# Kernel tuning notes

Measured on AMD Instinct MI355X. Metric: run time of the kernel, lower is better.

The kernel has to match this reference:

```python
import jax, jax.numpy as jnp
import numpy as np

N_NODES = 100000
N_EDGES = 10000
N_PAIRS = 1600000
F = 128


def setup_inputs() -> dict:
    key = jax.random.key(0)
    ks = jax.random.split(key, 7)
    x = jax.random.normal(ks[0], (N_NODES, F), dtype=jnp.float32)
    action = jax.random.uniform(ks[1], (N_NODES, 3), dtype=jnp.float32)
    W_msg = jax.random.normal(ks[2], (F, F), dtype=jnp.float32) * (1.0 / np.sqrt(F))
    W_upd = jax.random.normal(ks[3], (F, F), dtype=jnp.float32) * (1.0 / np.sqrt(F))
    b_upd = jax.random.normal(ks[4], (F,), dtype=jnp.float32) * 0.02
    pair_node = jax.random.randint(ks[5], (N_PAIRS,), 0, N_NODES, dtype=jnp.int32)
    pair_edge = jax.random.randint(ks[6], (N_PAIRS,), 0, N_EDGES, dtype=jnp.int32)
    return {"x": x, "action": action, "W_msg": W_msg, "W_upd": W_upd,
            "b_upd": b_upd, "pair_node": pair_node, "pair_edge": pair_edge}


def _v2v_mean(m, pair_node, pair_edge):
    # v2e: mean of incident node features per hyperedge, then
    # e2v: mean of incident hyperedge features per node.
    ones = jnp.ones((pair_node.shape[0],), dtype=m.dtype)
    edge_deg = jax.ops.segment_sum(ones, pair_edge, num_segments=N_EDGES)
    node_deg = jax.ops.segment_sum(ones, pair_node, num_segments=N_NODES)
    # gather node features to incidence pairs, reduce into edges  [E, F]
    e_feat = jax.ops.segment_sum(m[pair_node], pair_edge, num_segments=N_EDGES)
    e_feat = e_feat / jnp.maximum(edge_deg, 1.0)[:, None]
    # gather edge features back to pairs, reduce into nodes       [N, F]
    v_feat = jax.ops.segment_sum(e_feat[pair_edge], pair_node, num_segments=N_NODES)
    v_feat = v_feat / jnp.maximum(node_deg, 1.0)[:, None]
    return v_feat


def reference(x, action, W_msg, W_upd, b_upd, pair_node, pair_edge):
    send = action[:, 0] + action[:, 2]      # [N]
    receive = action[:, 0] + action[:, 1]   # [N]
    m_ji = x @ W_msg.T                       # lin_message (no bias)
    m_ji = jax.nn.gelu(m_ji, approximate=False)  # dropout=0 (eval)
    m_ji = m_ji * send[:, None]
    m_i = _v2v_mean(m_ji, pair_node, pair_edge)
    m_i = m_i * receive[:, None]
    h_i = jax.nn.gelu(x @ W_upd.T + b_upd + m_i, approximate=False)
    return h_i
```

## Files before the change

### kernel.cpp

```cpp
#include <hip/hip_runtime.h>

#define N_NODESC 100000
#define N_EDGESC 10000
#define N_PAIRSC 1600000
#define FDIM 128

#define NB 200
#define EPB 50
#define NPB 500
#define ECAP2 8704
#define PA_CHUNK 8192
#define PA_NCH ((N_PAIRSC + PA_CHUNK - 1) / PA_CHUNK)

typedef short bf16x8 __attribute__((ext_vector_type(8)));
typedef float f32x4 __attribute__((ext_vector_type(4)));
typedef float f32x2 __attribute__((ext_vector_type(2)));
typedef int i32x4 __attribute__((ext_vector_type(4)));
typedef unsigned u32x4 __attribute__((ext_vector_type(4)));

__device__ __forceinline__ unsigned short f2b(float f) {
  unsigned u = __float_as_uint(f);
  u += 0x7fffu + ((u >> 16) & 1u);
  return (unsigned short)(u >> 16);
}
__device__ __forceinline__ float b2f(unsigned short b) {
  return __uint_as_float(((unsigned)b) << 16);
}
__device__ __forceinline__ unsigned pack2(float a, float b) {
  return (unsigned)f2b(a) | ((unsigned)f2b(b) << 16);
}
__device__ __forceinline__ float gelu_fast(float z) {
  float z2 = z * z;
  float w = fmaf(0.044715f, z2, 1.0f);
  float e = __expf(1.5957691216f * z * w);
  return z * e * __builtin_amdgcn_rcpf(e + 1.0f);
}
__device__ __forceinline__ bf16x8 ldA(const float* p) {
  float4 u0 = *(const float4*)p;
  float4 u1 = *(const float4*)(p + 4);
  u32x4 w = {pack2(u0.x, u0.y), pack2(u0.z, u0.w), pack2(u1.x, u1.y), pack2(u1.z, u1.w)};
  return __builtin_bit_cast(bf16x8, w);
}

__global__ __launch_bounds__(256) void k_prep(const float* __restrict__ action,
                                              const float* __restrict__ wmsg, const float* __restrict__ wupd,
                                              short* __restrict__ wmsgb, short* __restrict__ wupdb,
                                              float* __restrict__ send, float* __restrict__ recv,
                                              int* __restrict__ gcure, int* __restrict__ gcurn) {
  int i = blockIdx.x * 256 + threadIdx.x;
  if (i < FDIM * FDIM) {
    wmsgb[i] = (short)f2b(wmsg[i]);
    wupdb[i] = (short)f2b(wupd[i]);
  }
  if (i < N_NODESC) {
    float a0 = action[i * 3 + 0], a1 = action[i * 3 + 1], a2 = action[i * 3 + 2];
    send[i] = a0 + a2;
    recv[i] = a0 + a1;
  }
  if (i < NB) {
    gcure[i] = i * ECAP2;
    gcurn[i] = i * ECAP2;
  }
}

__device__ __forceinline__ int wave_incl_scan(int v, int lane) {
#pragma unroll
  for (int d = 1; d < 64; d <<= 1) {
    int n = __shfl_up(v, d, 64);
    if (lane >= d) v += n;
  }
  return v;
}

__global__ __launch_bounds__(256) void k_part(const int* __restrict__ pn, const int* __restrict__ pe,
                                              int* __restrict__ gcure, int* __restrict__ gcurn,
                                              unsigned* __restrict__ buckE,
                                              unsigned* __restrict__ buckN) {
  __shared__ int ce[NB], cn[NB];
  int t = threadIdx.x;
  for (int i = t; i < NB; i += 256) { ce[i] = 0; cn[i] = 0; }
  __syncthreads();
  long long base = (long long)blockIdx.x * PA_CHUNK;
  for (int q = t; q < PA_CHUNK / 4; q += 256) {
    long long idx = base + (long long)q * 4;
    if (idx >= N_PAIRSC) break;
    i32x4 e4 = __builtin_nontemporal_load((const i32x4*)(pe + idx));
    i32x4 v4 = __builtin_nontemporal_load((const i32x4*)(pn + idx));
#pragma unroll
    for (int j = 0; j < 4; j++) {
      atomicAdd(&ce[e4[j] / EPB], 1);
      atomicAdd(&cn[v4[j] / NPB], 1);
    }
  }
  __syncthreads();
  for (int i = t; i < NB; i += 256) {
    ce[i] = atomicAdd(&gcure[i], ce[i]);
    cn[i] = atomicAdd(&gcurn[i], cn[i]);
  }
  __syncthreads();
  for (int q = t; q < PA_CHUNK / 4; q += 256) {
    long long idx = base + (long long)q * 4;
    if (idx >= N_PAIRSC) break;
    i32x4 e4 = __builtin_nontemporal_load((const i32x4*)(pe + idx));
    i32x4 v4 = __builtin_nontemporal_load((const i32x4*)(pn + idx));
#pragma unroll
    for (int j = 0; j < 4; j++) {
      unsigned ee = (unsigned)e4[j], vv = (unsigned)v4[j];
      int p1 = atomicAdd(&ce[ee / EPB], 1);
      buckE[p1] = (ee << 17) | vv;
      int p2 = atomicAdd(&cn[vv / NPB], 1);
      buckN[p2] = (vv << 14) | ee;
    }
  }
}

__global__ __launch_bounds__(256) void k_fine(const unsigned* __restrict__ buckE,
                                              const unsigned* __restrict__ buckN,
                                              const int* __restrict__ gcure, const int* __restrict__ gcurn,
                                              int* __restrict__ ecnt, int* __restrict__ eoff,
                                              int* __restrict__ ncnt, int* __restrict__ noff,
                                              int* __restrict__ sn, int* __restrict__ se) {
  __shared__ int cnt_s[NPB], cur_s[NPB];
  int b = blockIdx.x, t = threadIdx.x;
  const unsigned* buck;
  int *kcnt, *koff, *out;
  int keys, lo, beg, end, shift, mask;
  if (b < NB) {
    buck = buckE; kcnt = ecnt; koff = eoff; out = sn;
    keys = EPB; lo = b * EPB; beg = b * ECAP2; end = gcure[b];
    shift = 17; mask = 0x1FFFF;
  } else {
    int bb = b - NB;
    buck = buckN; kcnt = ncnt; koff = noff; out = se;
    keys = NPB; lo = bb * NPB; beg = bb * ECAP2; end = gcurn[bb];
    shift = 14; mask = 0x3FFF;
  }
  for (int i = t; i < keys; i += 256) cnt_s[i] = 0;
  __syncthreads();
  for (int i = beg + t; i < end; i += 256) {
    int key = (int)(buck[i] >> shift) - lo;
    atomicAdd(&cnt_s[key], 1);
  }
  __syncthreads();
  if (t < 64) {
    int carry = beg;
    for (int base = 0; base < keys; base += 64) {
      int idx = base + t;
      int v = (idx < keys) ? cnt_s[idx] : 0;
      int inc = wave_incl_scan(v, t);
      if (idx < keys) cur_s[idx] = carry + inc - v;
      carry += __shfl(inc, 63, 64);
    }
  }
  __syncthreads();
  for (int i = t; i < keys; i += 256) {
    kcnt[lo + i] = cnt_s[i];
    koff[lo + i] = cur_s[i];
  }
  __syncthreads();
  for (int i = beg + t; i < end; i += 256) {
    unsigned u = buck[i];
    int key = (int)(u >> shift) - lo;
    int val = (int)(u & mask);
    int pos = atomicAdd(&cur_s[key], 1);
    out[pos] = val;
  }
}

__global__ __launch_bounds__(256) void k_gemm_msg(const float* __restrict__ x, const short* __restrict__ wb,
                                                  const float* __restrict__ send,
                                                  unsigned char* __restrict__ mji8) {
  int gw = (blockIdx.x * 256 + threadIdx.x) >> 6;
  int lane = threadIdx.x & 63;
  if (gw >= N_NODESC / 32) return;
  int rb = gw * 32;
  int lr = lane & 15, lg = lane >> 4;

  bf16x8 A0[4], A1[4];
  const float* xrow0 = x + (size_t)(rb + lr) * FDIM + lg * 8;
  const float* xrow1 = xrow0 + 16 * FDIM;
#pragma unroll
  for (int kk = 0; kk < 4; kk++) {
    A0[kk] = ldA(xrow0 + kk * 32);
    A1[kk] = ldA(xrow1 + kk * 32);
  }

  float sv0[4], sv1[4];
#pragma unroll
  for (int j = 0; j < 4; j++) {
    sv0[j] = send[rb + lg * 4 + j];
    sv1[j] = send[rb + 16 + lg * 4 + j];
  }

#pragma unroll
  for (int c = 0; c < 8; c++) {
    f32x4 acc0 = {0.f, 0.f, 0.f, 0.f}, acc1 = {0.f, 0.f, 0.f, 0.f};
    const short* wrow = wb + (size_t)(16 * c + lr) * FDIM + lg * 8;
#pragma unroll
    for (int kk = 0; kk < 4; kk++) {
      bf16x8 B = *(const bf16x8*)(wrow + kk * 32);
      acc0 = __builtin_amdgcn_mfma_f32_16x16x32_bf16(A0[kk], B, acc0, 0, 0, 0);
      acc1 = __builtin_amdgcn_mfma_f32_16x16x32_bf16(A1[kk], B, acc1, 0, 0, 0);
    }
    int col = 16 * c + lr;
#pragma unroll
    for (int j = 0; j < 4; j++) {
      float m0 = gelu_fast(acc0[j]) * sv0[j];
      float m1 = gelu_fast(acc1[j]) * sv1[j];
      int row0 = rb + lg * 4 + j;
      mji8[(size_t)row0 * FDIM + col] =
          (unsigned char)(__builtin_amdgcn_cvt_pk_fp8_f32(m0, m0, 0, false) & 0xFF);
      mji8[(size_t)(row0 + 16) * FDIM + col] =
          (unsigned char)(__builtin_amdgcn_cvt_pk_fp8_f32(m1, m1, 0, false) & 0xFF);
    }
  }
}

__global__ __launch_bounds__(256) void k_edge(const unsigned char* __restrict__ mji8, const int* __restrict__ sn,
                                              const int* __restrict__ eoff, const int* __restrict__ ecnt,
                                              unsigned char* __restrict__ efeat8) {
  int wave = blockIdx.x * 4 + (threadIdx.x >> 6);
  int lane = threadIdx.x & 63;
  int half = lane >> 5;
  int sub2 = (lane >> 4) & 1;
  int c4 = lane & 15;
  int edge = wave * 2 + half;
  if (edge >= N_EDGESC) return;
  int beg = eoff[edge], cnt = ecnt[edge];
  f32x2 a0 = {0.f, 0.f}, a1 = {0.f, 0.f}, a2 = {0.f, 0.f}, a3 = {0.f, 0.f};
#pragma unroll 4
  for (int p = sub2; p < cnt; p += 2) {
    int node = sn[beg + p];
    uint2 u = ((const uint2*)(mji8 + (size_t)node * FDIM))[c4];
    a0 += __builtin_amdgcn_cvt_pk_f32_fp8(u.x, false);
    a1 += __builtin_amdgcn_cvt_pk_f32_fp8(u.x, true);
    a2 += __builtin_amdgcn_cvt_pk_f32_fp8(u.y, false);
    a3 += __builtin_amdgcn_cvt_pk_f32_fp8(u.y, true);
  }
  a0[0] += __shfl_xor(a0[0], 16, 64); a0[1] += __shfl_xor(a0[1], 16, 64);
  a1[0] += __shfl_xor(a1[0], 16, 64); a1[1] += __shfl_xor(a1[1], 16, 64);
  a2[0] += __shfl_xor(a2[0], 16, 64); a2[1] += __shfl_xor(a2[1], 16, 64);
  a3[0] += __shfl_xor(a3[0], 16, 64); a3[1] += __shfl_xor(a3[1], 16, 64);
  if (sub2 == 0) {
    float inv = 1.0f / fmaxf((float)cnt, 1.0f);
    uint2 o;
    o.x = (unsigned)__builtin_amdgcn_cvt_pk_fp8_f32(a0[0] * inv, a0[1] * inv, 0, false);
    o.x = (unsigned)__builtin_amdgcn_cvt_pk_fp8_f32(a1[0] * inv, a1[1] * inv, (int)o.x, true);
    o.y = (unsigned)__builtin_amdgcn_cvt_pk_fp8_f32(a2[0] * inv, a2[1] * inv, 0, false);
    o.y = (unsigned)__builtin_amdgcn_cvt_pk_fp8_f32(a3[0] * inv, a3[1] * inv, (int)o.y, true);
    ((uint2*)(efeat8 + (size_t)edge * FDIM))[c4] = o;
  }
}

__global__ __launch_bounds__(256) void k_node(const unsigned char* __restrict__ efeat8, const int* __restrict__ se,
                                              const int* __restrict__ noff, const int* __restrict__ ncnt,
                                              const float* __restrict__ recv, short* __restrict__ mi) {
  int wave = blockIdx.x * 4 + (threadIdx.x >> 6);
  int lane = threadIdx.x & 63;
  int sub = lane >> 4, c4 = lane & 15;
  int node = wave * 4 + sub;
  int beg = noff[node], cnt = ncnt[node];
  f32x2 a0 = {0.f, 0.f}, a1 = {0.f, 0.f}, a2 = {0.f, 0.f}, a3 = {0.f, 0.f};
#pragma unroll 4
  for (int p = 0; p < cnt; p++) {
    int e = se[beg + p];
    uint2 u = ((const uint2*)(efeat8 + (size_t)e * FDIM))[c4];
    a0 += __builtin_amdgcn_cvt_pk_f32_fp8(u.x, false);
    a1 += __builtin_amdgcn_cvt_pk_f32_fp8(u.x, true);
    a2 += __builtin_amdgcn_cvt_pk_f32_fp8(u.y, false);
    a3 += __builtin_amdgcn_cvt_pk_f32_fp8(u.y, true);
  }
  float s = recv[node] / fmaxf((float)cnt, 1.0f);
  u32x4 o;
  o[0] = pack2(a0[0] * s, a0[1] * s);
  o[1] = pack2(a1[0] * s, a1[1] * s);
  o[2] = pack2(a2[0] * s, a2[1] * s);
  o[3] = pack2(a3[0] * s, a3[1] * s);
  ((u32x4*)(mi + (size_t)node * FDIM))[c4] = o;
}

__global__ __launch_bounds__(256) void k_gemm_upd(const float* __restrict__ x, const short* __restrict__ wb,
                                                  const float* __restrict__ bias, const short* __restrict__ mi,
                                                  float* __restrict__ out) {
  int gw = (blockIdx.x * 256 + threadIdx.x) >> 6;
  int lane = threadIdx.x & 63;
  if (gw >= N_NODESC / 32) return;
  int rb = gw * 32;
  int lr = lane & 15, lg = lane >> 4;

  bf16x8 A0[4], A1[4];
  const float* xrow0 = x + (size_t)(rb + lr) * FDIM + lg * 8;
  const float* xrow1 = xrow0 + 16 * FDIM;
#pragma unroll
  for (int kk = 0; kk < 4; kk++) {
    A0[kk] = ldA(xrow0 + kk * 32);
    A1[kk] = ldA(xrow1 + kk * 32);
  }

#pragma unroll
  for (int c = 0; c < 8; c++) {
    f32x4 acc0 = {0.f, 0.f, 0.f, 0.f}, acc1 = {0.f, 0.f, 0.f, 0.f};
    const short* wrow = wb + (size_t)(16 * c + lr) * FDIM + lg * 8;
#pragma unroll
    for (int kk = 0; kk < 4; kk++) {
      bf16x8 B = *(const bf16x8*)(wrow + kk * 32);
      acc0 = __builtin_amdgcn_mfma_f32_16x16x32_bf16(A0[kk], B, acc0, 0, 0, 0);
      acc1 = __builtin_amdgcn_mfma_f32_16x16x32_bf16(A1[kk], B, acc1, 0, 0, 0);
    }
    int col = 16 * c + lr;
    float bc = bias[col];
#pragma unroll
    for (int j = 0; j < 4; j++) {
      int row0 = rb + lg * 4 + j;
      float z0 = acc0[j] + bc + b2f(((const unsigned short*)mi)[(size_t)row0 * FDIM + col]);
      float z1 = acc1[j] + bc + b2f(((const unsigned short*)mi)[(size_t)(row0 + 16) * FDIM + col]);
      __builtin_nontemporal_store(gelu_fast(z0), &out[(size_t)row0 * FDIM + col]);
      __builtin_nontemporal_store(gelu_fast(z1), &out[(size_t)(row0 + 16) * FDIM + col]);
    }
  }
}

extern "C" void kernel_launch(void* const* d_in, const int* in_sizes, int n_in,
                              void* d_out, int out_size, void* d_ws, size_t ws_size,
                              hipStream_t stream) {
  const float* x = (const float*)d_in[0];
  const float* action = (const float*)d_in[1];
  const float* wmsg = (const float*)d_in[2];
  const float* wupd = (const float*)d_in[3];
  const float* bupd = (const float*)d_in[4];
  const int* pn = (const int*)d_in[5];
  const int* pe = (const int*)d_in[6];
  float* out = (float*)d_out;

  char* p = (char*)d_ws;
  auto alloc = [&](size_t bytes) -> char* {
    char* r = p;
    p += (bytes + 255) & ~(size_t)255;
    return r;
  };
  unsigned char* mji8 = (unsigned char*)alloc((size_t)N_NODESC * FDIM);
  short* mi = (short*)alloc((size_t)N_NODESC * FDIM * 2);
  unsigned char* efeat8 = (unsigned char*)alloc((size_t)N_EDGESC * FDIM);
  int* sn = (int*)alloc((size_t)NB * ECAP2 * 4);
  int* se = (int*)alloc((size_t)NB * ECAP2 * 4);
  short* wmsgb = (short*)alloc(FDIM * FDIM * 2);
  short* wupdb = (short*)alloc(FDIM * FDIM * 2);
  float* send = (float*)alloc(N_NODESC * 4);
  float* recv = (float*)alloc(N_NODESC * 4);
  int* ecnt = (int*)alloc(N_EDGESC * 4);
  int* eoff = (int*)alloc(N_EDGESC * 4);
  int* ncnt = (int*)alloc(N_NODESC * 4);
  int* noff = (int*)alloc(N_NODESC * 4);
  int* gcure = (int*)alloc(NB * 4);
  int* gcurn = (int*)alloc(NB * 4);

  unsigned* buckE = (unsigned*)mi;
  unsigned* buckN = buckE + (size_t)NB * ECAP2;

  k_prep<<<391, 256, 0, stream>>>(action, wmsg, wupd, wmsgb, wupdb, send, recv, gcure, gcurn);
  k_part<<<PA_NCH, 256, 0, stream>>>(pn, pe, gcure, gcurn, buckE, buckN);
  k_fine<<<2 * NB, 256, 0, stream>>>(buckE, buckN, gcure, gcurn, ecnt, eoff, ncnt, noff, sn, se);
  k_gemm_msg<<<782, 256, 0, stream>>>(x, wmsgb, send, mji8);
  k_edge<<<1250, 256, 0, stream>>>(mji8, sn, eoff, ecnt, efeat8);
  k_node<<<6250, 256, 0, stream>>>(efeat8, se, noff, ncnt, recv, mi);
  k_gemm_upd<<<782, 256, 0, stream>>>(x, wupdb, bupd, mi, out);
}
```

Measured before the change: 184.9 us.

## Merge independent stages into shared launches to overlap partitioning with GEMM and aggregation

Independent work is merged into single launches. The pair partitioning kernel now shares a grid with the message GEMM, and the node-side fine sort shares a grid with the edge aggregation. The edge-side fine sort becomes its own small kernel so that the edge aggregation only waits on it. The goal is to cut launch gaps and tail underutilisation by running latency-bound atomics alongside compute-heavy blocks. The cost is more register and shared-memory pressure in the heterogeneous kernels, which may lower occupancy.

```diff
diff --git a/kernel.cpp b/kernel.cpp
--- a/kernel.cpp
+++ b/kernel.cpp
@@ -11,6 +11,7 @@
 #define ECAP2 8704
 #define PA_CHUNK 8192
 #define PA_NCH ((N_PAIRSC + PA_CHUNK - 1) / PA_CHUNK)
+#define MSG_BLKS 782
 
 typedef short bf16x8 __attribute__((ext_vector_type(8)));
 typedef float f32x4 __attribute__((ext_vector_type(4)));
@@ -72,183 +73,197 @@
   return v;
 }
 
-__global__ __launch_bounds__(256) void k_part(const int* __restrict__ pn, const int* __restrict__ pe,
-                                              int* __restrict__ gcure, int* __restrict__ gcurn,
-                                              unsigned* __restrict__ buckE,
-                                              unsigned* __restrict__ buckN) {
+__global__ __launch_bounds__(256) void k_part_msg(const int* __restrict__ pn, const int* __restrict__ pe,
+                                                  int* __restrict__ gcure, int* __restrict__ gcurn,
+                                                  unsigned* __restrict__ buckE, unsigned* __restrict__ buckN,
+                                                  const float* __restrict__ x, const short* __restrict__ wb,
+                                                  const float* __restrict__ send,
+                                                  unsigned char* __restrict__ mji8) {
   __shared__ int ce[NB], cn[NB];
   int t = threadIdx.x;
-  for (int i = t; i < NB; i += 256) { ce[i] = 0; cn[i] = 0; }
+  if (blockIdx.x < PA_NCH) {
+    for (int i = t; i < NB; i += 256) { ce[i] = 0; cn[i] = 0; }
+    __syncthreads();
+    long long base = (long long)blockIdx.x * PA_CHUNK;
+    for (int q = t; q < PA_CHUNK / 4; q += 256) {
+      long long idx = base + (long long)q * 4;
+      if (idx >= N_PAIRSC) break;
+      i32x4 e4 = __builtin_nontemporal_load((const i32x4*)(pe + idx));
+      i32x4 v4 = __builtin_nontemporal_load((const i32x4*)(pn + idx));
+#pragma unroll
+      for (int j = 0; j < 4; j++) {
+        atomicAdd(&ce[e4[j] / EPB], 1);
+        atomicAdd(&cn[v4[j] / NPB], 1);
+      }
+    }
+    __syncthreads();
+    for (int i = t; i < NB; i += 256) {
+      ce[i] = atomicAdd(&gcure[i], ce[i]);
+      cn[i] = atomicAdd(&gcurn[i], cn[i]);
+    }
+    __syncthreads();
+    for (int q = t; q < PA_CHUNK / 4; q += 256) {
+      long long idx = base + (long long)q * 4;
+      if (idx >= N_PAIRSC) break;
+      i32x4 e4 = __builtin_nontemporal_load((const i32x4*)(pe + idx));
+      i32x4 v4 = __builtin_nontemporal_load((const i32x4*)(pn + idx));
+#pragma unroll
+      for (int j = 0; j < 4; j++) {
+        unsigned ee = (unsigned)e4[j], vv = (unsigned)v4[j];
+        int p1 = atomicAdd(&ce[ee / EPB], 1);
+        buckE[p1] = (ee << 17) | vv;
+        int p2 = atomicAdd(&cn[vv / NPB], 1);
+        buckN[p2] = (vv << 14) | ee;
+      }
+    }
+  } else {
+    int gw = ((int)(blockIdx.x - PA_NCH) * 256 + t) >> 6;
+    int lane = t & 63;
+    if (gw >= N_NODESC / 32) return;
+    int rb = gw * 32;
+    int lr = lane & 15, lg = lane >> 4;
+
+    bf16x8 A0[4], A1[4];
+    const float* xrow0 = x + (size_t)(rb + lr) * FDIM + lg * 8;
+    const float* xrow1 = xrow0 + 16 * FDIM;
+#pragma unroll
+    for (int kk = 0; kk < 4; kk++) {
+      A0[kk] = ldA(xrow0 + kk * 32);
+      A1[kk] = ldA(xrow1 + kk * 32);
+    }
+    float sv0[4], sv1[4];
+#pragma unroll
+    for (int j = 0; j < 4; j++) {
+      sv0[j] = send[rb + lg * 4 + j];
+      sv1[j] = send[rb + 16 + lg * 4 + j];
+    }
+#pragma unroll
+    for (int c = 0; c < 8; c++) {
+      f32x4 acc0 = {0.f, 0.f, 0.f, 0.f}, acc1 = {0.f, 0.f, 0.f, 0.f};
+      const short* wrow = wb + (size_t)(16 * c + lr) * FDIM + lg * 8;
+#pragma unroll
+      for (int kk = 0; kk < 4; kk++) {
+        bf16x8 B = *(const bf16x8*)(wrow + kk * 32);
+        acc0 = __builtin_amdgcn_mfma_f32_16x16x32_bf16(A0[kk], B, acc0, 0, 0, 0);
+        acc1 = __builtin_amdgcn_mfma_f32_16x16x32_bf16(A1[kk], B, acc1, 0, 0, 0);
+      }
+      int col = 16 * c + lr;
+#pragma unroll
+      for (int j = 0; j < 4; j++) {
+        float m0 = gelu_fast(acc0[j]) * sv0[j];
+        float m1 = gelu_fast(acc1[j]) * sv1[j];
+        int row0 = rb + lg * 4 + j;
+        mji8[(size_t)row0 * FDIM + col] =
+            (unsigned char)(__builtin_amdgcn_cvt_pk_fp8_f32(m0, m0, 0, false) & 0xFF);
+        mji8[(size_t)(row0 + 16) * FDIM + col] =
+            (unsigned char)(__builtin_amdgcn_cvt_pk_fp8_f32(m1, m1, 0, false) & 0xFF);
+      }
+    }
+  }
+}
+
+__global__ __launch_bounds__(256) void k_fine_e(const unsigned* __restrict__ buckE,
+                                                const int* __restrict__ gcure,
+                                                int* __restrict__ ecnt, int* __restrict__ eoff,
+                                                int* __restrict__ sn) {
+  __shared__ int cnt_s[EPB], cur_s[EPB];
+  int b = blockIdx.x, t = threadIdx.x;
+  int lo = b * EPB, beg = b * ECAP2, end = gcure[b];
+  if (t < EPB) cnt_s[t] = 0;
   __syncthreads();
-  long long base = (long long)blockIdx.x * PA_CHUNK;
-  for (int q = t; q < PA_CHUNK / 4; q += 256) {
-    long long idx = base + (long long)q * 4;
-    if (idx >= N_PAIRSC) break;
-    i32x4 e4 = __builtin_nontemporal_load((const i32x4*)(pe + idx));
-    i32x4 v4 = __builtin_nontemporal_load((const i32x4*)(pn + idx));
-#pragma unroll
-    for (int j = 0; j < 4; j++) {
-      atomicAdd(&ce[e4[j] / EPB], 1);
-      atomicAdd(&cn[v4[j] / NPB], 1);
-    }
-  }
+  for (int i = beg + t; i < end; i += 256)
+    atomicAdd(&cnt_s[(int)(buckE[i] >> 17) - lo], 1);
   __syncthreads();
-  for (int i = t; i < NB; i += 256) {
-    ce[i] = atomicAdd(&gcure[i], ce[i]);
-    cn[i] = atomicAdd(&gcurn[i], cn[i]);
+  if (t < 64) {
+    int v = (t < EPB) ? cnt_s[t] : 0;
+    int inc = wave_incl_scan(v, t);
+    if (t < EPB) cur_s[t] = beg + inc - v;
   }
   __syncthreads();
-  for (int q = t; q < PA_CHUNK / 4; q += 256) {
-    long long idx = base + (long long)q * 4;
-    if (idx >= N_PAIRSC) break;
-    i32x4 e4 = __builtin_nontemporal_load((const i32x4*)(pe + idx));
-    i32x4 v4 = __builtin_nontemporal_load((const i32x4*)(pn + idx));
-#pragma unroll
-    for (int j = 0; j < 4; j++) {
-      unsigned ee = (unsigned)e4[j], vv = (unsigned)v4[j];
-      int p1 = atomicAdd(&ce[ee / EPB], 1);
-      buckE[p1] = (ee << 17) | vv;
-      int p2 = atomicAdd(&cn[vv / NPB], 1);
-      buckN[p2] = (vv << 14) | ee;
-    }
-  }
-}
-
-__global__ __launch_bounds__(256) void k_fine(const unsigned* __restrict__ buckE,
-                                              const unsigned* __restrict__ buckN,
-                                              const int* __restrict__ gcure, const int* __restrict__ gcurn,
-                                              int* __restrict__ ecnt, int* __restrict__ eoff,
-                                              int* __restrict__ ncnt, int* __restrict__ noff,
-                                              int* __restrict__ sn, int* __restrict__ se) {
-  __shared__ int cnt_s[NPB], cur_s[NPB];
-  int b = blockIdx.x, t = threadIdx.x;
-  const unsigned* buck;
-  int *kcnt, *koff, *out;
-  int keys, lo, beg, end, shift, mask;
-  if (b < NB) {
-    buck = buckE; kcnt = ecnt; koff = eoff; out = sn;
-    keys = EPB; lo = b * EPB; beg = b * ECAP2; end = gcure[b];
-    shift = 17; mask = 0x1FFFF;
-  } else {
-    int bb = b - NB;
-    buck = buckN; kcnt = ncnt; koff = noff; out = se;
-    keys = NPB; lo = bb * NPB; beg = bb * ECAP2; end = gcurn[bb];
-    shift = 14; mask = 0x3FFF;
-  }
-  for (int i = t; i < keys; i += 256) cnt_s[i] = 0;
+  if (t < EPB) {
+    ecnt[lo + t] = cnt_s[t];
+    eoff[lo + t] = cur_s[t];
+  }
   __syncthreads();
   for (int i = beg + t; i < end; i += 256) {
-    int key = (int)(buck[i] >> shift) - lo;
-    atomicAdd(&cnt_s[key], 1);
-  }
-  __syncthreads();
-  if (t < 64) {
-    int carry = beg;
-    for (int base = 0; base < keys; base += 64) {
-      int idx = base + t;
-      int v = (idx < keys) ? cnt_s[idx] : 0;
-      int inc = wave_incl_scan(v, t);
-      if (idx < keys) cur_s[idx] = carry + inc - v;
-      carry += __shfl(inc, 63, 64);
-    }
-  }
-  __syncthreads();
-  for (int i = t; i < keys; i += 256) {
-    kcnt[lo + i] = cnt_s[i];
-    koff[lo + i] = cur_s[i];
-  }
-  __syncthreads();
-  for (int i = beg + t; i < end; i += 256) {
-    unsigned u = buck[i];
-    int key = (int)(u >> shift) - lo;
-    int val = (int)(u & mask);
+    unsigned u = buckE[i];
+    int key = (int)(u >> 17) - lo;
     int pos = atomicAdd(&cur_s[key], 1);
-    out[pos] = val;
-  }
-}
-
-__global__ __launch_bounds__(256) void k_gemm_msg(const float* __restrict__ x, const short* __restrict__ wb,
-                                                  const float* __restrict__ send,
-                                                  unsigned char* __restrict__ mji8) {
-  int gw = (blockIdx.x * 256 + threadIdx.x) >> 6;
-  int lane = threadIdx.x & 63;
-  if (gw >= N_NODESC / 32) return;
-  int rb = gw * 32;
-  int lr = lane & 15, lg = lane >> 4;
-
-  bf16x8 A0[4], A1[4];
-  const float* xrow0 = x + (size_t)(rb + lr) * FDIM + lg * 8;
-  const float* xrow1 = xrow0 + 16 * FDIM;
-#pragma unroll
-  for (int kk = 0; kk < 4; kk++) {
-    A0[kk] = ldA(xrow0 + kk * 32);
-    A1[kk] = ldA(xrow1 + kk * 32);
-  }
-
-  float sv0[4], sv1[4];
-#pragma unroll
-  for (int j = 0; j < 4; j++) {
-    sv0[j] = send[rb + lg * 4 + j];
-    sv1[j] = send[rb + 16 + lg * 4 + j];
-  }
-
-#pragma unroll
-  for (int c = 0; c < 8; c++) {
-    f32x4 acc0 = {0.f, 0.f, 0.f, 0.f}, acc1 = {0.f, 0.f, 0.f, 0.f};
-    const short* wrow = wb + (size_t)(16 * c + lr) * FDIM + lg * 8;
-#pragma unroll
-    for (int kk = 0; kk < 4; kk++) {
-      bf16x8 B = *(const bf16x8*)(wrow + kk * 32);
-      acc0 = __builtin_amdgcn_mfma_f32_16x16x32_bf16(A0[kk], B, acc0, 0, 0, 0);
-      acc1 = __builtin_amdgcn_mfma_f32_16x16x32_bf16(A1[kk], B, acc1, 0, 0, 0);
-    }
-    int col = 16 * c + lr;
-#pragma unroll
-    for (int j = 0; j < 4; j++) {
-      float m0 = gelu_fast(acc0[j]) * sv0[j];
-      float m1 = gelu_fast(acc1[j]) * sv1[j];
-      int row0 = rb + lg * 4 + j;
-      mji8[(size_t)row0 * FDIM + col] =
-          (unsigned char)(__builtin_amdgcn_cvt_pk_fp8_f32(m0, m0, 0, false) & 0xFF);
-      mji8[(size_t)(row0 + 16) * FDIM + col] =
-          (unsigned char)(__builtin_amdgcn_cvt_pk_fp8_f32(m1, m1, 0, false) & 0xFF);
-    }
-  }
-}
-
-__global__ __launch_bounds__(256) void k_edge(const unsigned char* __restrict__ mji8, const int* __restrict__ sn,
-                                              const int* __restrict__ eoff, const int* __restrict__ ecnt,
-                                              unsigned char* __restrict__ efeat8) {
-  int wave = blockIdx.x * 4 + (threadIdx.x >> 6);
-  int lane = threadIdx.x & 63;
-  int half = lane >> 5;
-  int sub2 = (lane >> 4) & 1;
-  int c4 = lane & 15;
-  int edge = wave * 2 + half;
-  if (edge >= N_EDGESC) return;
-  int beg = eoff[edge], cnt = ecnt[edge];
-  f32x2 a0 = {0.f, 0.f}, a1 = {0.f, 0.f}, a2 = {0.f, 0.f}, a3 = {0.f, 0.f};
+    sn[pos] = (int)(u & 0x1FFFF);
+  }
+}
+
+__global__ __launch_bounds__(256) void k_edge_fineN(const unsigned* __restrict__ buckN,
+                                                    const int* __restrict__ gcurn,
+                                                    int* __restrict__ ncnt, int* __restrict__ noff,
+                                                    int* __restrict__ se,
+                                                    const unsigned char* __restrict__ mji8,
+                                                    const int* __restrict__ sn,
+                                                    const int* __restrict__ eoff, const int* __restrict__ ecnt,
+                                                    unsigned char* __restrict__ efeat8) {
+  __shared__ int cnt_s[NPB], cur_s[NPB];
+  int t = threadIdx.x;
+  if (blockIdx.x < NB) {
+    int b = blockIdx.x;
+    int lo = b * NPB, beg = b * ECAP2, end = gcurn[b];
+    for (int i = t; i < NPB; i += 256) cnt_s[i] = 0;
+    __syncthreads();
+    for (int i = beg + t; i < end; i += 256)
+      atomicAdd(&cnt_s[(int)(buckN[i] >> 14) - lo], 1);
+    __syncthreads();
+    if (t < 64) {
+      int carry = beg;
+#pragma unroll
+      for (int base = 0; base < NPB; base += 64) {
+        int idx = base + t;
+        int v = (idx < NPB) ? cnt_s[idx] : 0;
+        int inc = wave_incl_scan(v, t);
+        if (idx < NPB) cur_s[idx] = carry + inc - v;
+        carry += __shfl(inc, 63, 64);
+      }
+    }
+    __syncthreads();
+    for (int i = t; i < NPB; i += 256) {
+      ncnt[lo + i] = cnt_s[i];
+      noff[lo + i] = cur_s[i];
+    }
+    __syncthreads();
+    for (int i = beg + t; i < end; i += 256) {
+      unsigned u = buckN[i];
+      int key = (int)(u >> 14) - lo;
+      int pos = atomicAdd(&cur_s[key], 1);
+      se[pos] = (int)(u & 0x3FFF);
+    }
+  } else {
+    int wave = (int)(blockIdx.x - NB) * 4 + (t >> 6);
+    int lane = t & 63;
+    int half = lane >> 5, sub2 = (lane >> 4) & 1, c4 = lane & 15;
+    int edge = wave * 2 + half;
+    if (edge >= N_EDGESC) return;
+    int beg = eoff[edge], cnt = ecnt[edge];
+    f32x2 a0 = {0.f, 0.f}, a1 = {0.f, 0.f}, a2 = {0.f, 0.f}, a3 = {0.f, 0.f};
 #pragma unroll 4
-  for (int p = sub2; p < cnt; p += 2) {
-    int node = sn[beg + p];
-    uint2 u = ((const uint2*)(mji8 + (size_t)node * FDIM))[c4];
-    a0 += __builtin_amdgcn_cvt_pk_f32_fp8(u.x, false);
-    a1 += __builtin_amdgcn_cvt_pk_f32_fp8(u.x, true);
-    a2 += __builtin_amdgcn_cvt_pk_f32_fp8(u.y, false);
-    a3 += __builtin_amdgcn_cvt_pk_f32_fp8(u.y, true);
-  }
-  a0[0] += __shfl_xor(a0[0], 16, 64); a0[1] += __shfl_xor(a0[1], 16, 64);
-  a1[0] += __shfl_xor(a1[0], 16, 64); a1[1] += __shfl_xor(a1[1], 16, 64);
-  a2[0] += __shfl_xor(a2[0], 16, 64); a2[1] += __shfl_xor(a2[1], 16, 64);
-  a3[0] += __shfl_xor(a3[0], 16, 64); a3[1] += __shfl_xor(a3[1], 16, 64);
-  if (sub2 == 0) {
-    float inv = 1.0f / fmaxf((float)cnt, 1.0f);
-    uint2 o;
-    o.x = (unsigned)__builtin_amdgcn_cvt_pk_fp8_f32(a0[0] * inv, a0[1] * inv, 0, false);
-    o.x = (unsigned)__builtin_amdgcn_cvt_pk_fp8_f32(a1[0] * inv, a1[1] * inv, (int)o.x, true);
-    o.y = (unsigned)__builtin_amdgcn_cvt_pk_fp8_f32(a2[0] * inv, a2[1] * inv, 0, false);
-    o.y = (unsigned)__builtin_amdgcn_cvt_pk_fp8_f32(a3[0] * inv, a3[1] * inv, (int)o.y, true);
-    ((uint2*)(efeat8 + (size_t)edge * FDIM))[c4] = o;
+    for (int p = sub2; p < cnt; p += 2) {
+      int node = sn[beg + p];
+      uint2 u = ((const uint2*)(mji8 + (size_t)node * FDIM))[c4];
+      a0 += __builtin_amdgcn_cvt_pk_f32_fp8(u.x, false);
+      a1 += __builtin_amdgcn_cvt_pk_f32_fp8(u.x, true);
+      a2 += __builtin_amdgcn_cvt_pk_f32_fp8(u.y, false);
+      a3 += __builtin_amdgcn_cvt_pk_f32_fp8(u.y, true);
+    }
+    a0[0] += __shfl_xor(a0[0], 16, 64); a0[1] += __shfl_xor(a0[1], 16, 64);
+    a1[0] += __shfl_xor(a1[0], 16, 64); a1[1] += __shfl_xor(a1[1], 16, 64);
+    a2[0] += __shfl_xor(a2[0], 16, 64); a2[1] += __shfl_xor(a2[1], 16, 64);
+    a3[0] += __shfl_xor(a3[0], 16, 64); a3[1] += __shfl_xor(a3[1], 16, 64);
+    if (sub2 == 0) {
+      float inv = 1.0f / fmaxf((float)cnt, 1.0f);
+      uint2 o;
+      o.x = (unsigned)__builtin_amdgcn_cvt_pk_fp8_f32(a0[0] * inv, a0[1] * inv, 0, false);
+      o.x = (unsigned)__builtin_amdgcn_cvt_pk_fp8_f32(a1[0] * inv, a1[1] * inv, (int)o.x, true);
+      o.y = (unsigned)__builtin_amdgcn_cvt_pk_fp8_f32(a2[0] * inv, a2[1] * inv, 0, false);
+      o.y = (unsigned)__builtin_amdgcn_cvt_pk_fp8_f32(a3[0] * inv, a3[1] * inv, (int)o.y, true);
+      ((uint2*)(efeat8 + (size_t)edge * FDIM))[c4] = o;
+    }
   }
 }
 
@@ -358,10 +373,11 @@
   unsigned* buckN = buckE + (size_t)NB * ECAP2;
 
   k_prep<<<391, 256, 0, stream>>>(action, wmsg, wupd, wmsgb, wupdb, send, recv, gcure, gcurn);
-  k_part<<<PA_NCH, 256, 0, stream>>>(pn, pe, gcure, gcurn, buckE, buckN);
-  k_fine<<<2 * NB, 256, 0, stream>>>(buckE, buckN, gcure, gcurn, ecnt, eoff, ncnt, noff, sn, se);
-  k_gemm_msg<<<782, 256, 0, stream>>>(x, wmsgb, send, mji8);
-  k_edge<<<1250, 256, 0, stream>>>(mji8, sn, eoff, ecnt, efeat8);
+  k_part_msg<<<PA_NCH + MSG_BLKS, 256, 0, stream>>>(pn, pe, gcure, gcurn, buckE, buckN,
+                                                    x, wmsgb, send, mji8);
+  k_fine_e<<<NB, 256, 0, stream>>>(buckE, gcure, ecnt, eoff, sn);
+  k_edge_fineN<<<NB + 1250, 256, 0, stream>>>(buckN, gcurn, ncnt, noff, se,
+                                              mji8, sn, eoff, ecnt, efeat8);
   k_node<<<6250, 256, 0, stream>>>(efeat8, se, noff, ncnt, recv, mi);
   k_gemm_upd<<<782, 256, 0, stream>>>(x, wupdb, bupd, mi, out);
 }
```

After: 175.5 us. -5.1%, faster.
